# Performance work log

Hardware: AMD Instinct MI355X
Metric: run time of the kernel (lower is better)

Reference implementation:

```python
import jax, jax.numpy as jnp
import numpy as np

N, C, H, W = 128, 3, 256, 256


def setup_inputs() -> dict:
    key = jax.random.key(0)
    k1, k2 = jax.random.split(key)
    inputs = jax.random.normal(k1, (N, C, H, W), dtype=jnp.float32)
    u = jax.random.uniform(k2, (N, 4), dtype=jnp.float32)
    # realistic crop params: scales in (0.3, 1.0], translations in (-0.2, 0.2)
    whbias = jnp.concatenate([0.3 + 0.7 * u[:, :2], 0.4 * u[:, 2:] - 0.2], axis=1)
    return {"inputs": inputs, "whbias": whbias}


def _reflect_clip(x, size):
    # PyTorch grid_sample padding_mode='reflection', align_corners=False:
    # reflect unnormalized coords about [-0.5, size-0.5], then clip to [0, size-1]
    span = float(size)
    x = jnp.abs(x + 0.5) % (2.0 * span)
    x = jnp.where(x > span, 2.0 * span - x, x) - 0.5
    return jnp.clip(x, 0.0, size - 1.0)


def _resized_crop(inputs, whbias):
    n, c, h, w = inputs.shape
    dt = inputs.dtype
    # F.affine_grid base coords, align_corners=False: centers of pixels in [-1, 1]
    xs = (jnp.arange(w, dtype=dt) + 0.5) * (2.0 / w) - 1.0  # [W]
    ys = (jnp.arange(h, dtype=dt) + 0.5) * (2.0 / h) - 1.0  # [H]
    w_s, h_s, w_b, h_b = whbias[:, 0], whbias[:, 1], whbias[:, 2], whbias[:, 3]
    # theta is diagonal + translation -> grid separable in x and y
    gx = w_s[:, None, None] * xs[None, None, :] + w_b[:, None, None]  # [N,H,W]
    gy = h_s[:, None, None] * ys[None, :, None] + h_b[:, None, None]  # [N,H,W]
    # unnormalize (align_corners=False): ix = ((gx+1)*W - 1)/2
    ix = _reflect_clip(((gx + 1.0) * w - 1.0) * 0.5, w)
    iy = _reflect_clip(((gy + 1.0) * h - 1.0) * 0.5, h)
    ix0 = jnp.floor(ix)
    iy0 = jnp.floor(iy)
    wx = (ix - ix0)[:, None]  # [N,1,H,W]
    wy = (iy - iy0)[:, None]
    ix0i = jnp.clip(ix0.astype(jnp.int32), 0, w - 1)
    ix1i = jnp.clip(ix0i + 1, 0, w - 1)
    iy0i = jnp.clip(iy0.astype(jnp.int32), 0, h - 1)
    iy1i = jnp.clip(iy0i + 1, 0, h - 1)

    def gather(img, yy, xx):  # img [C,H,W], yy/xx [H,W] -> [C,H,W]
        return img[:, yy, xx]

    g = jax.vmap(gather)
    v00 = g(inputs, iy0i, ix0i)
    v01 = g(inputs, iy0i, ix1i)
    v10 = g(inputs, iy1i, ix0i)
    v11 = g(inputs, iy1i, ix1i)
    # bilinear blend
    return (v00 * (1.0 - wx) * (1.0 - wy) + v01 * wx * (1.0 - wy)
            + v10 * (1.0 - wx) * wy + v11 * wx * wy)


def reference(inputs, whbias):
    # size=None -> no adaptive_avg_pool2d; output is [N,C,H,W]
    return _resized_crop(inputs, whbias)
```

## Files before the change

### kernel.cpp

```cpp
#include <hip/hip_runtime.h>


constexpr int N_ = 128, C_ = 3, H_ = 256, W_ = 256, HW_ = H_ * W_;
constexpr int SEG_ = 264;

typedef float f32x4 __attribute__((ext_vector_type(4)));

__device__ __forceinline__ void coord(float scale, float bias, float xf, int size,
                                      int& i0, float& w) {
    const float span = (float)size;
    const float two  = 2.0f * span;
    float xs  = (xf + 0.5f) * (2.0f / span) - 1.0f;
    float g   = scale * xs + bias;
    float pre = ((g + 1.0f) * span - 1.0f) * 0.5f;
    float t = fabsf(pre + 0.5f);
    t = t - two * floorf(t * (1.0f / two));
    t = (t > span) ? (two - t) : t;
    t -= 0.5f;
    t = fminf(fmaxf(t, 0.0f), span - 1.0f);
    float f = floorf(t);
    w  = t - f;
    i0 = (int)f;
}

__global__ __launch_bounds__(256)
void rrc_kernel(const float* __restrict__ in, const float* __restrict__ wh,
                float* __restrict__ out) {
    __shared__ float V[4 * C_ * SEG_];
    const int n   = blockIdx.x >> 6;
    const int ys  = (blockIdx.x & 63) * 4;
    const int tid = threadIdx.x;
    const int xq  = tid & 63;
    const int yl  = tid >> 6;

    const float w_s = wh[n * 4 + 0];
    const float h_s = wh[n * 4 + 1];
    const float w_b = wh[n * 4 + 2];
    const float h_b = wh[n * 4 + 3];

    int iy0; float wy;
    coord(h_s, h_b, (float)(ys + yl), H_, iy0, wy);
    const int iy1 = min(iy0 + 1, H_ - 1);

    int offA[4], offB[4]; float wx[4];
#pragma unroll
    for (int j = 0; j < 4; ++j) {
        int i0;
        coord(w_s, w_b, (float)(xq * 4 + j), W_, i0, wx[j]);
        const int xb = min(i0 + 1, W_ - 1);
        offA[j] = i0 + (i0 >> 5);
        offB[j] = xb + (xb >> 5);
    }

    const float* __restrict__ inN = in + (size_t)n * C_ * HW_;
    f32x4 g0[C_], g1[C_];
#pragma unroll
    for (int c = 0; c < C_; ++c) {
        g0[c] = *reinterpret_cast<const f32x4*>(inN + c * HW_ + iy0 * W_ + xq * 4);
        g1[c] = *reinterpret_cast<const f32x4*>(inN + c * HW_ + iy1 * W_ + xq * 4);
    }

    float* __restrict__ outN = out + (size_t)n * C_ * HW_;
    const int segBase = yl * C_ * SEG_;
    const int woff    = xq * 4 + (xq >> 3);

#pragma unroll
    for (int c = 0; c < C_; ++c) {
        const f32x4 v = g0[c] + wy * (g1[c] - g0[c]);
        float* seg = &V[segBase + c * SEG_];
        *reinterpret_cast<f32x4*>(seg + woff) = v;
        f32x4 o;
#pragma unroll
        for (int j = 0; j < 4; ++j) {
            const float a = seg[offA[j]];
            const float b = seg[offB[j]];
            o[j] = a + wx[j] * (b - a);
        }
        *reinterpret_cast<f32x4*>(outN + (c * H_ + ys + yl) * W_ + xq * 4) = o;
    }
}

extern "C" void kernel_launch(void* const* d_in, const int* in_sizes, int n_in,
                              void* d_out, int out_size, void* d_ws, size_t ws_size,
                              hipStream_t stream) {
    const float* in = (const float*)d_in[0];
    const float* wh = (const float*)d_in[1];
    float* out      = (float*)d_out;
    (void)in_sizes; (void)n_in; (void)out_size; (void)d_ws; (void)ws_size;

    dim3 grid(N_ * 64);
    dim3 block(256);
    rrc_kernel<<<grid, block, 0, stream>>>(in, wh, out);
}
```

Baseline: 34.34 us.

## Process four row groups per block with register prefetch of next rows

Each block now handles four strided row groups instead of one, cutting the grid by four. The input rows for the next group are loaded into registers while the current group is blended and written. Output stores become nontemporal. This amortizes per-block setup such as the x-coordinate math and hides load latency. The cost is more registers and fewer blocks in flight, which reduces parallelism.

```diff
diff --git a/kernel.cpp b/kernel.cpp
--- a/kernel.cpp
+++ b/kernel.cpp
@@ -27,8 +27,8 @@
 void rrc_kernel(const float* __restrict__ in, const float* __restrict__ wh,
                 float* __restrict__ out) {
     __shared__ float V[4 * C_ * SEG_];
-    const int n   = blockIdx.x >> 6;
-    const int ys  = (blockIdx.x & 63) * 4;
+    const int n   = blockIdx.x >> 4;
+    const int s0  = blockIdx.x & 15;
     const int tid = threadIdx.x;
     const int xq  = tid & 63;
     const int yl  = tid >> 6;
@@ -37,10 +37,6 @@
     const float h_s = wh[n * 4 + 1];
     const float w_b = wh[n * 4 + 2];
     const float h_b = wh[n * 4 + 3];
-
-    int iy0; float wy;
-    coord(h_s, h_b, (float)(ys + yl), H_, iy0, wy);
-    const int iy1 = min(iy0 + 1, H_ - 1);
 
     int offA[4], offB[4]; float wx[4];
 #pragma unroll
@@ -52,31 +48,66 @@
         offB[j] = xb + (xb >> 5);
     }
 
-    const float* __restrict__ inN = in + (size_t)n * C_ * HW_;
-    f32x4 g0[C_], g1[C_];
+    const float* __restrict__ inN  = in  + (size_t)n * C_ * HW_;
+    float* __restrict__       outN = out + (size_t)n * C_ * HW_;
+    const int sx   = xq * 4;
+    const int woff = sx + (xq >> 3);
+    float* const seg0 = &V[(yl * C_ + 0) * SEG_];
+    float* const seg1 = &V[(yl * C_ + 1) * SEG_];
+    float* const seg2 = &V[(yl * C_ + 2) * SEG_];
+
+    int cy0; float cwy;
+    coord(h_s, h_b, (float)(s0 * 4 + yl), H_, cy0, cwy);
+    int cy1 = min(cy0 + 1, H_ - 1);
+    f32x4 c0[C_], c1[C_], p0[C_], p1[C_];
 #pragma unroll
     for (int c = 0; c < C_; ++c) {
-        g0[c] = *reinterpret_cast<const f32x4*>(inN + c * HW_ + iy0 * W_ + xq * 4);
-        g1[c] = *reinterpret_cast<const f32x4*>(inN + c * HW_ + iy1 * W_ + xq * 4);
+        c0[c] = *reinterpret_cast<const f32x4*>(inN + c * HW_ + cy0 * W_ + sx);
+        c1[c] = *reinterpret_cast<const f32x4*>(inN + c * HW_ + cy1 * W_ + sx);
     }
 
-    float* __restrict__ outN = out + (size_t)n * C_ * HW_;
-    const int segBase = yl * C_ * SEG_;
-    const int woff    = xq * 4 + (xq >> 3);
+#pragma unroll
+    for (int i = 0; i < 4; ++i) {
+        int ny0 = 0, ny1 = 0; float nwy = 0.0f;
+        if (i < 3) {
+            coord(h_s, h_b, (float)((s0 + 16 * (i + 1)) * 4 + yl), H_, ny0, nwy);
+            ny1 = min(ny0 + 1, H_ - 1);
+#pragma unroll
+            for (int c = 0; c < C_; ++c) {
+                p0[c] = *reinterpret_cast<const f32x4*>(inN + c * HW_ + ny0 * W_ + sx);
+                p1[c] = *reinterpret_cast<const f32x4*>(inN + c * HW_ + ny1 * W_ + sx);
+            }
+        }
 
+        {
+            const f32x4 v0 = c0[0] + cwy * (c1[0] - c0[0]);
+            const f32x4 v1 = c0[1] + cwy * (c1[1] - c0[1]);
+            const f32x4 v2 = c0[2] + cwy * (c1[2] - c0[2]);
+            *reinterpret_cast<f32x4*>(seg0 + woff) = v0;
+            *reinterpret_cast<f32x4*>(seg1 + woff) = v1;
+            *reinterpret_cast<f32x4*>(seg2 + woff) = v2;
+        }
+
+        const int y = (s0 + 16 * i) * 4 + yl;
 #pragma unroll
-    for (int c = 0; c < C_; ++c) {
-        const f32x4 v = g0[c] + wy * (g1[c] - g0[c]);
-        float* seg = &V[segBase + c * SEG_];
-        *reinterpret_cast<f32x4*>(seg + woff) = v;
-        f32x4 o;
+        for (int c = 0; c < C_; ++c) {
+            float* const seg = (c == 0) ? seg0 : (c == 1) ? seg1 : seg2;
+            f32x4 o;
 #pragma unroll
-        for (int j = 0; j < 4; ++j) {
-            const float a = seg[offA[j]];
-            const float b = seg[offB[j]];
-            o[j] = a + wx[j] * (b - a);
+            for (int j = 0; j < 4; ++j) {
+                const float a = seg[offA[j]];
+                const float b = seg[offB[j]];
+                o[j] = a + wx[j] * (b - a);
+            }
+            __builtin_nontemporal_store(o, reinterpret_cast<f32x4*>(
+                outN + (c * H_ + y) * W_ + sx));
         }
-        *reinterpret_cast<f32x4*>(outN + (c * H_ + ys + yl) * W_ + xq * 4) = o;
+
+        if (i < 3) {
+            cy0 = ny0; cy1 = ny1; cwy = nwy;
+#pragma unroll
+            for (int c = 0; c < C_; ++c) { c0[c] = p0[c]; c1[c] = p1[c]; }
+        }
     }
 }
 
@@ -88,7 +119,7 @@
     float* out      = (float*)d_out;
     (void)in_sizes; (void)n_in; (void)out_size; (void)d_ws; (void)ws_size;
 
-    dim3 grid(N_ * 64);
+    dim3 grid(N_ * 16);
     dim3 block(256);
     rrc_kernel<<<grid, block, 0, stream>>>(in, wh, out);
 }
```

New measurement: 35.66 us. +3.8%, slower.
